# Optimization experiments

Hardware: AMD Instinct MI355X
Metric: run time of the kernel (lower is better)

The kernel has to match this reference:

```python
import jax, jax.numpy as jnp
import numpy as np

EPS = 1e-6

def _conv1x1(x, w, bias):
    # x: [b,cin,h,w], w: [cout,cin]
    y = jnp.einsum('bchw,oc->bohw', x, w)
    return y + bias[None, :, None, None]

def _maxpool2(x):
    b, c, h, w = x.shape
    return x.reshape(b, c, h // 2, 2, w // 2, 2).max(axis=(3, 5))

def _up2_align_corners(x):
    # bilinear upsample x2, align_corners=True (matches torch nn.Upsample)
    b, c, h, w = x.shape
    oh, ow = 2 * h, 2 * w
    ys = jnp.linspace(0.0, h - 1.0, oh)
    xs = jnp.linspace(0.0, w - 1.0, ow)
    y0 = jnp.floor(ys).astype(jnp.int32); y1 = jnp.minimum(y0 + 1, h - 1)
    x0 = jnp.floor(xs).astype(jnp.int32); x1 = jnp.minimum(x0 + 1, w - 1)
    ty = (ys - y0).reshape(1, 1, oh, 1)
    tx = (xs - x0).reshape(1, 1, 1, ow)
    r0 = x[:, :, y0, :]; r1 = x[:, :, y1, :]           # [b,c,oh,w]
    v00 = r0[:, :, :, x0]; v01 = r0[:, :, :, x1]       # [b,c,oh,ow]
    v10 = r1[:, :, :, x0]; v11 = r1[:, :, :, x1]
    return (1 - ty) * ((1 - tx) * v00 + tx * v01) + ty * ((1 - tx) * v10 + tx * v11)

def _norm_corr(fm):
    # fm: [b,N,N], indexed [b,p,q]; ReLU then L2-normalize over q for each p
    m = jnp.maximum(fm, 0.0)
    norm = jnp.sqrt(jnp.sum(m * m, axis=2, keepdims=True) + EPS)
    return m / norm

def setup_inputs() -> dict:
    key = jax.random.key(0)
    ks = jax.random.split(key, 8)
    d = {
        'xa': jax.random.normal(ks[0], (8, 256, 64, 64), jnp.float32),
        'xb': jax.random.normal(ks[1], (8, 256, 64, 64), jnp.float32),
        'conv_w': jax.random.normal(ks[2], (1024, 256), jnp.float32) * 0.02,
        'conv_b': jax.random.normal(ks[3], (1024,), jnp.float32) * 0.02,
        'We': jax.random.normal(ks[4], (1024, 1024), jnp.float32) * 0.02,
        'We2': jax.random.normal(ks[5], (1024, 1024), jnp.float32) * 0.02,
        'conv2_w': jax.random.normal(ks[6], (256, 1024), jnp.float32) * 0.02,
        'conv2_b': jax.random.normal(ks[7], (256,), jnp.float32) * 0.02,
    }
    return d

def reference(xa, xb, conv_w, conv_b, We, We2, conv2_w, conv2_b):
    fa = _maxpool2(_conv1x1(xa, conv_w, conv_b))   # [b,c,h,w]
    fb = _maxpool2(_conv1x1(xb, conv_w, conv_b))
    b, c, h, w = fa.shape
    N = h * w
    Fa = fa.reshape(b, c, N)                        # [b,c,N]
    Fb = fb.reshape(b, c, N)
    Fb_t = jnp.swapaxes(Fb, 1, 2)                   # [b,N,c]
    Fa_t = jnp.swapaxes(Fa, 1, 2)
    # fm[b,p,q] = (linear_e(Fb_t) @ Fa)
    fm = jnp.einsum('bpc,cd,bdq->bpq', Fb_t, We.T, Fa)
    Mab = _norm_corr(fm)                            # normalized over q per p
    fm2 = jnp.einsum('bpc,cd,bdq->bpq', Fa_t, We2.T, Fb)
    Mba = _norm_corr(fm2)
    # torch: bmm(corr.view(b,N,N), feat) with corr_flat[b,q,p] = Mn[b,p,q]
    en_a = jnp.einsum('bpq,bpk->bqk', Mab, Fa_t)    # [b,N,c]
    en_b = jnp.einsum('bpq,bpk->bqk', Mba, Fb_t)
    # faithful reinterpretation (torch .view(b,c,h,w) on a [b,N,c] tensor)
    en_a = en_a.reshape(b, c, h, w)
    en_b = en_b.reshape(b, c, h, w)
    en_a = _conv1x1(_up2_align_corners(en_a), conv2_w, conv2_b)
    en_b = _conv1x1(_up2_align_corners(en_b), conv2_w, conv2_b)
    return (en_a, en_b)
```

## Files before the change

kernel.cpp:

```cpp
#include <hip/hip_runtime.h>

typedef unsigned short u16;
typedef short bfrag __attribute__((ext_vector_type(8)));
typedef float facc  __attribute__((ext_vector_type(4)));

__device__ __forceinline__ float bf2f(u16 u) {
    union { unsigned int i; float f; } v; v.i = ((unsigned int)u) << 16; return v.f;
}
__device__ __forceinline__ u16 f2bf(float f) {
    union { float f; unsigned int i; } v; v.f = f;
    unsigned int r = v.i + 0x7FFFu + ((v.i >> 16) & 1u);
    return (u16)(r >> 16);
}

__device__ __forceinline__ void store_out(u16* p, float v)   { *p = f2bf(v); }
__device__ __forceinline__ void store_out(float* p, float v) { *p = v; }

__device__ __forceinline__ void gl2lds16(const u16* g, char* l) {
    __builtin_amdgcn_global_load_lds(
        (const __attribute__((address_space(1))) unsigned int*)g,
        (__attribute__((address_space(3))) unsigned int*)l,
        16, 0, 0);
}

__global__ void cvt4_k(const float* __restrict__ s0, u16* __restrict__ d0,
                       const float* __restrict__ s1, u16* __restrict__ d1,
                       const float* __restrict__ s2, u16* __restrict__ d2,
                       const float* __restrict__ s3, u16* __restrict__ d3) {
    int i = blockIdx.x * blockDim.x + threadIdx.x;
    if (i < 262144)        d0[i] = f2bf(s0[i]);
    else if (i < 1310720)  d1[i - 262144] = f2bf(s1[i - 262144]);
    else if (i < 2359296)  d2[i - 1310720] = f2bf(s2[i - 1310720]);
    else                   d3[i - 2359296] = f2bf(s3[i - 2359296]);
}

__global__ void transpose_in_k(const float* __restrict__ srcA,
                               const float* __restrict__ srcB,
                               u16* __restrict__ dst) {
    __shared__ u16 tile[64][65];
    const long SX = 1048576;
    const int z  = blockIdx.z;
    const int c0 = blockIdx.x * 64;
    const int r0 = blockIdx.y * 64;
    const int x  = threadIdx.x;
    const int y0 = threadIdx.y;
    const float* s = (z < 8 ? srcA : srcB) + (size_t)(z & 7) * SX;
    for (int i = 0; i < 8; ++i) {
        int r = y0 + i * 8;
        tile[r][x] = f2bf(s[(size_t)(r0 + r) * 4096 + c0 + x]);
    }
    __syncthreads();
    u16* d = dst + (size_t)z * SX;
    for (int i = 0; i < 8; ++i) {
        int c = y0 + i * 8;
        d[(size_t)(c0 + c) * 256 + r0 + x] = tile[x][c];
    }
}

template <typename OutT, int MODE, bool PAIRED>
__global__ __launch_bounds__(256)
void gemm_nt(const u16* __restrict__ A0, const u16* __restrict__ A1, long strideA,
             const u16* __restrict__ B0, const u16* __restrict__ B1, long strideBT,
             OutT* __restrict__ C, long strideC, u16* __restrict__ CT,
             const float* __restrict__ bias, int M, int N, int K) {
    constexpr bool POOL    = (MODE == 2);
    constexpr int  SMEM_SZ = POOL ? 33792 : 32768;
    __shared__ __align__(16) char smem[SMEM_SZ];
    char* As = smem;
    char* Bs = smem + 16384;

    const int gx = gridDim.x, gy = gridDim.y;
    long id = blockIdx.x + (long)gx * (blockIdx.y + (long)gy * blockIdx.z);
    long total = (long)gx * gy * gridDim.z;
    long nid = (id & 7) * (total >> 3) + (id >> 3);
    const int bx = (int)(nid % gx);
    long rr = nid / gx;
    const int by = (int)(rr % gy);
    const int b  = (int)(rr / gy);

    const int m0 = bx * 128;
    const int n0 = by * 128;

    const u16* Ab; const u16* Bb;
    if (PAIRED) {
        const int bl = b & 7;
        Ab = (b < 8 ? A0 : A1) + (size_t)bl * strideA;
        Bb = (b < 8 ? B0 : B1) + (size_t)bl * strideBT;
    } else {
        Ab = A0 + (size_t)b * strideA;
        Bb = B0 + (size_t)b * strideBT;
    }

    const int t    = threadIdx.x;
    const int lane = t & 63;
    const int w    = t >> 6;
    const int wm   = (w & 1) * 64;
    const int wn   = (w >> 1) * 64;
    const int q    = lane >> 4;
    const int ln   = lane & 15;

    const int s0 = w * 64 + lane;
    const int s1 = s0 + 256;
    const int r0s = s0 >> 2, c0s = (s0 & 3) * 8;
    const int r1s = s1 >> 2, c1s = (s1 & 3) * 8;

    const u16* pA0 = Ab + (size_t)(m0 + r0s) * K + c0s;
    const u16* pA1 = Ab + (size_t)(m0 + r1s) * K + c1s;
    const u16* pB0 = Bb + (size_t)(n0 + r0s) * K + c0s;
    const u16* pB1 = Bb + (size_t)(n0 + r1s) * K + c1s;

    facc acc[4][4];
    for (int i = 0; i < 4; ++i)
        for (int j = 0; j < 4; ++j)
            acc[i][j] = (facc)0.0f;

    const int nK = K >> 6;
    for (int kt = 0; kt < nK; ++kt) {
        const int k0 = kt << 6;
        gl2lds16(pA0 + k0,      As + s0 * 16);
        gl2lds16(pA1 + k0,      As + s1 * 16);
        gl2lds16(pA0 + k0 + 32, As + 8192 + s0 * 16);
        gl2lds16(pA1 + k0 + 32, As + 8192 + s1 * 16);
        gl2lds16(pB0 + k0,      Bs + s0 * 16);
        gl2lds16(pB1 + k0,      Bs + s1 * 16);
        gl2lds16(pB0 + k0 + 32, Bs + 8192 + s0 * 16);
        gl2lds16(pB1 + k0 + 32, Bs + 8192 + s1 * 16);
        __syncthreads();
        for (int j = 0; j < 2; ++j) {
            const char* Aj = As + j * 8192;
            const char* Bj = Bs + j * 8192;
            bfrag af[4], bfr[4];
            for (int mt = 0; mt < 4; ++mt)
                af[mt] = *reinterpret_cast<const bfrag*>(Aj + (wm + mt * 16 + ln) * 64 + q * 16);
            for (int nt = 0; nt < 4; ++nt)
                bfr[nt] = *reinterpret_cast<const bfrag*>(Bj + (wn + nt * 16 + ln) * 64 + q * 16);
            for (int mt = 0; mt < 4; ++mt)
                for (int nt = 0; nt < 4; ++nt)
                    acc[mt][nt] = __builtin_amdgcn_mfma_f32_16x16x32_bf16(af[mt], bfr[nt], acc[mt][nt], 0, 0, 0);
        }
        __syncthreads();
    }

    if (POOL) {
        u16* Cp  = (u16*)C + (size_t)b * strideC;
        float* pool0 = (float*)smem;
        float* pool1 = (float*)(smem + 16896);
        float* pb = (w >> 1) ? pool1 : pool0;
        for (int mt = 0; mt < 4; ++mt) {
            for (int nt = 0; nt < 4; ++nt) {
                for (int r = 0; r < 4; ++r) {
                    int ch = wm + mt * 16 + q * 4 + r;
                    float v = acc[mt][nt][r] + bias[m0 + ch];
                    float vm = fmaxf(v, __shfl_xor(v, 1, 64));
                    if (!(ln & 1))
                        pb[ch * 33 + ((nt * 16 + ln) >> 1)] = vm;
                }
            }
        }
        __syncthreads();
        for (int i = 0; i < 8; ++i) {
            int idx = t + i * 256;
            int ch = idx >> 4, xpp = (idx & 15) * 2;
            float v0 = fmaxf(pool0[ch * 33 + xpp],     pool1[ch * 33 + xpp]);
            float v1 = fmaxf(pool0[ch * 33 + xpp + 1], pool1[ch * 33 + xpp + 1]);
            unsigned pk = (unsigned)f2bf(v0) | ((unsigned)f2bf(v1) << 16);
            *reinterpret_cast<unsigned*>(&Cp[(size_t)(m0 + ch) * 1024 + by * 32 + xpp]) = pk;
            pool0[ch * 33 + xpp] = v0; pool0[ch * 33 + xpp + 1] = v1;
        }
        __syncthreads();
        u16* CTb = CT + (size_t)b * strideC;
        for (int i = 0; i < 8; ++i) {
            int idx = t + i * 256;
            int ch2 = (idx & 63) * 2, xp = idx >> 6;
            unsigned pk = (unsigned)f2bf(pool0[ch2 * 33 + xp]) |
                          ((unsigned)f2bf(pool0[(ch2 + 1) * 33 + xp]) << 16);
            *reinterpret_cast<unsigned*>(&CTb[(size_t)(by * 32 + xp) * 1024 + m0 + ch2]) = pk;
        }
    } else if (MODE == 0) {
        u16* Cb = (u16*)C + (size_t)b * strideC;
        u16* dump = (u16*)smem;
        for (int mt = 0; mt < 4; ++mt)
            for (int nt = 0; nt < 4; ++nt)
                for (int r = 0; r < 4; ++r)
                    dump[(wm + mt * 16 + q * 4 + r) * 128 + wn + nt * 16 + ln] = f2bf(acc[mt][nt][r]);
        __syncthreads();
        for (int i = 0; i < 8; ++i) {
            const int row = w * 32 + i * 4 + (lane >> 4);
            const uint4 v = *reinterpret_cast<const uint4*>(dump + row * 128 + (lane & 15) * 8);
            *reinterpret_cast<uint4*>(Cb + (size_t)(m0 + row) * N + n0 + (lane & 15) * 8) = v;
        }
    } else {
        OutT* Cb = C + (size_t)b * strideC;
        for (int mt = 0; mt < 4; ++mt) {
            const int rbase = m0 + wm + mt * 16 + q * 4;
            for (int nt = 0; nt < 4; ++nt) {
                const int col = n0 + wn + nt * 16 + ln;
                for (int r = 0; r < 4; ++r)
                    store_out(&Cb[(size_t)(rbase + r) * N + col], acc[mt][nt][r] + bias[rbase + r]);
            }
        }
    }
}

__global__ void norm_rk(const u16* __restrict__ fm, float* __restrict__ rinv) {
    __shared__ float red[4];
    const long row = blockIdx.x;
    const u16* p = fm + row * 1024;
    const int t = threadIdx.x;
    uint2 raw = *reinterpret_cast<const uint2*>(p + t * 4);
    float v0 = fmaxf(bf2f((u16)(raw.x & 0xFFFF)), 0.f);
    float v1 = fmaxf(bf2f((u16)(raw.x >> 16)), 0.f);
    float v2 = fmaxf(bf2f((u16)(raw.y & 0xFFFF)), 0.f);
    float v3 = fmaxf(bf2f((u16)(raw.y >> 16)), 0.f);
    float s = v0 * v0 + v1 * v1 + v2 * v2 + v3 * v3;
    for (int off = 32; off; off >>= 1) s += __shfl_down(s, off, 64);
    if ((t & 63) == 0) red[t >> 6] = s;
    __syncthreads();
    if (t == 0)
        rinv[row] = 1.0f / sqrtf(red[0] + red[1] + red[2] + red[3] + 1e-6f);
}

__global__ void transpose_scale_k(const u16* __restrict__ src,
                                  const float* __restrict__ rinv,
                                  u16* __restrict__ dst) {
    __shared__ u16 tile[64][65];
    const long S = 1048576;
    const int b  = blockIdx.z;
    const int c0 = blockIdx.x * 64;
    const int r0 = blockIdx.y * 64;
    const int x  = threadIdx.x;
    const int y0 = threadIdx.y;
    const u16* s = src + (size_t)b * S;
    const float* rv = rinv + (size_t)b * 1024;
    for (int i = 0; i < 8; ++i) {
        int r = y0 + i * 8;
        float v = fmaxf(bf2f(s[(size_t)(r0 + r) * 1024 + c0 + x]), 0.f) * rv[r0 + r];
        tile[r][x] = f2bf(v);
    }
    __syncthreads();
    u16* d = dst + (size_t)b * S;
    for (int i = 0; i < 8; ++i) {
        int c = y0 + i * 8;
        d[(size_t)(c0 + c) * 1024 + r0 + x] = tile[x][c];
    }
}

__global__ void upsample_k(const float* __restrict__ V, float* __restrict__ out, int total) {
    int idx = blockIdx.x * blockDim.x + threadIdx.x;
    if (idx >= total) return;
    int X  = idx & 63;
    int Y  = (idx >> 6) & 63;
    long bo = idx >> 12;
    const float* p = V + bo * 1024;
    const float sc = 31.0f / 63.0f;
    float ys = Y * sc;
    float xs = X * sc;
    int y0 = (int)ys; int x0 = (int)xs;
    int y1 = y0 + 1; if (y1 > 31) y1 = 31;
    int x1 = x0 + 1; if (x1 > 31) x1 = 31;
    float ty = ys - y0, tx = xs - x0;
    float v00 = p[y0 * 32 + x0], v01 = p[y0 * 32 + x1];
    float v10 = p[y1 * 32 + x0], v11 = p[y1 * 32 + x1];
    out[idx] = (1.f - ty) * ((1.f - tx) * v00 + tx * v01) + ty * ((1.f - tx) * v10 + tx * v11);
}

extern "C" void kernel_launch(void* const* d_in, const int* in_sizes, int n_in,
                              void* d_out, int out_size, void* d_ws, size_t ws_size,
                              hipStream_t stream) {
    const float* xa      = (const float*)d_in[0];
    const float* xb      = (const float*)d_in[1];
    const float* conv_w  = (const float*)d_in[2];
    const float* conv_b  = (const float*)d_in[3];
    const float* We      = (const float*)d_in[4];
    const float* We2     = (const float*)d_in[5];
    const float* conv2_w = (const float*)d_in[6];
    const float* conv2_b = (const float*)d_in[7];
    float* out = (float*)d_out;
    char* ws = (char*)d_ws;

    const long S1M = 1048576;
    const long MiB = 1048576;

    u16*   XT  = (u16*)(ws + 0);
    u16*   T1  = (u16*)(ws + 0);
    u16*   MT  = (u16*)(ws + 0);
    u16*   FA  = (u16*)(ws + 32 * MiB);
    u16*   FB  = (u16*)(ws + 48 * MiB);
    u16*   FAT = (u16*)(ws + 64 * MiB);
    u16*   FBT = (u16*)(ws + 80 * MiB);
    float* V   = (float*)(ws + 64 * MiB);
    u16*   FM  = (u16*)(ws + 96 * MiB);
    u16*   Z   = (u16*)(ws + 96 * MiB);
    u16*   CW  = (u16*)(ws + 128 * MiB);
    u16*   WE  = (u16*)(ws + 128 * MiB + 524288);
    u16*   WE2 = (u16*)(ws + 128 * MiB + 2621440);
    u16*   C2W = (u16*)(ws + 128 * MiB + 4718592);
    float* RIV = (float*)(ws + 128 * MiB + 5242880);

    const dim3 tb64(64, 8);

    cvt4_k<<<10240, 256, 0, stream>>>(conv_w, CW, We, WE, We2, WE2, conv2_w, C2W);

    transpose_in_k<<<dim3(64, 4, 16), tb64, 0, stream>>>(xa, xb, XT);

    gemm_nt<u16, 2, false><<<dim3(8, 32, 16), 256, 0, stream>>>(
        CW, CW, 0, XT, XT, S1M, FA, S1M, FAT, conv_b, 1024, 4096, 256);

    gemm_nt<u16, 0, true><<<dim3(8, 8, 16), 256, 0, stream>>>(
        FBT, FAT, S1M, WE, WE2, 0, T1, S1M, nullptr, nullptr, 1024, 1024, 1024);

    gemm_nt<u16, 0, true><<<dim3(8, 8, 16), 256, 0, stream>>>(
        T1, T1 + 8 * S1M, S1M, FAT, FBT, S1M, FM, S1M, nullptr, nullptr, 1024, 1024, 1024);

    norm_rk<<<16384, 256, 0, stream>>>(FM, RIV);

    transpose_scale_k<<<dim3(16, 16, 16), tb64, 0, stream>>>(FM, RIV, MT);

    gemm_nt<u16, 0, true><<<dim3(8, 8, 16), 256, 0, stream>>>(
        FA, FB, S1M, MT, MT + 8 * S1M, S1M, Z, S1M, nullptr, nullptr, 1024, 1024, 1024);

    gemm_nt<float, 1, false><<<dim3(2, 8, 16), 256, 0, stream>>>(
        C2W, C2W, 0, Z, Z, S1M, V, 256L * 1024, nullptr, conv2_b, 256, 1024, 1024);

    upsample_k<<<65536, 256, 0, stream>>>(V, out, 16 * 256 * 4096);
}
```

Before: 428.0 us.

## Reorder pooled-GEMM B rows so 2x2 maxpool reduces in registers via shuffles

In the fused conv+maxpool GEMM, the B-operand rows are now gathered in a permuted pixel order, so each 16-column MFMA tile holds complete 2x2 pooling windows. The pooling max is then done entirely with lane shuffles in registers, and the pooled output and its transposed copy are written straight from registers. This removes the LDS staging buffers, two block barriers and the extra shared memory in the pool epilogue. In exchange the stores become narrower and scattered (2-byte stores for C, 8-byte stores for CT), and the B loads now read non-contiguous rows.

```diff
diff --git a/kernel.cpp b/kernel.cpp
--- a/kernel.cpp
+++ b/kernel.cpp
@@ -63,9 +63,8 @@
              const u16* __restrict__ B0, const u16* __restrict__ B1, long strideBT,
              OutT* __restrict__ C, long strideC, u16* __restrict__ CT,
              const float* __restrict__ bias, int M, int N, int K) {
-    constexpr bool POOL    = (MODE == 2);
-    constexpr int  SMEM_SZ = POOL ? 33792 : 32768;
-    __shared__ __align__(16) char smem[SMEM_SZ];
+    constexpr bool POOL = (MODE == 2);
+    __shared__ __align__(16) char smem[32768];
     char* As = smem;
     char* Bs = smem + 16384;
 
@@ -104,10 +103,15 @@
     const int r0s = s0 >> 2, c0s = (s0 & 3) * 8;
     const int r1s = s1 >> 2, c1s = (s1 & 3) * 8;
 
+    const int gr0 = POOL ? ((2 * by + ((r0s >> 1) & 1)) * 64 + (r0s >> 2) * 2 + (r0s & 1))
+                         : (n0 + r0s);
+    const int gr1 = POOL ? ((2 * by + ((r1s >> 1) & 1)) * 64 + (r1s >> 2) * 2 + (r1s & 1))
+                         : (n0 + r1s);
+
     const u16* pA0 = Ab + (size_t)(m0 + r0s) * K + c0s;
     const u16* pA1 = Ab + (size_t)(m0 + r1s) * K + c1s;
-    const u16* pB0 = Bb + (size_t)(n0 + r0s) * K + c0s;
-    const u16* pB1 = Bb + (size_t)(n0 + r1s) * K + c1s;
+    const u16* pB0 = Bb + (size_t)gr0 * K + c0s;
+    const u16* pB1 = Bb + (size_t)gr1 * K + c1s;
 
     facc acc[4][4];
     for (int i = 0; i < 4; ++i)
@@ -143,38 +147,35 @@
 
     if (POOL) {
         u16* Cp  = (u16*)C + (size_t)b * strideC;
-        float* pool0 = (float*)smem;
-        float* pool1 = (float*)(smem + 16896);
-        float* pb = (w >> 1) ? pool1 : pool0;
+        u16* CTb = CT + (size_t)b * strideC;
+        const int a = ln >> 2;
         for (int mt = 0; mt < 4; ++mt) {
+            const int chb = wm + mt * 16 + q * 4;
+            float bs0 = bias[m0 + chb + 0];
+            float bs1 = bias[m0 + chb + 1];
+            float bs2 = bias[m0 + chb + 2];
+            float bs3 = bias[m0 + chb + 3];
             for (int nt = 0; nt < 4; ++nt) {
-                for (int r = 0; r < 4; ++r) {
-                    int ch = wm + mt * 16 + q * 4 + r;
-                    float v = acc[mt][nt][r] + bias[m0 + ch];
-                    float vm = fmaxf(v, __shfl_xor(v, 1, 64));
-                    if (!(ln & 1))
-                        pb[ch * 33 + ((nt * 16 + ln) >> 1)] = vm;
+                const int xp = (wn >> 2) + nt * 4 + a;
+                float p0 = acc[mt][nt][0] + bs0;
+                float p1 = acc[mt][nt][1] + bs1;
+                float p2 = acc[mt][nt][2] + bs2;
+                float p3 = acc[mt][nt][3] + bs3;
+                p0 = fmaxf(p0, __shfl_xor(p0, 1, 64)); p0 = fmaxf(p0, __shfl_xor(p0, 2, 64));
+                p1 = fmaxf(p1, __shfl_xor(p1, 1, 64)); p1 = fmaxf(p1, __shfl_xor(p1, 2, 64));
+                p2 = fmaxf(p2, __shfl_xor(p2, 1, 64)); p2 = fmaxf(p2, __shfl_xor(p2, 2, 64));
+                p3 = fmaxf(p3, __shfl_xor(p3, 1, 64)); p3 = fmaxf(p3, __shfl_xor(p3, 2, 64));
+                float s01 = (ln & 1) ? p1 : p0;
+                float s23 = (ln & 1) ? p3 : p2;
+                float sel = (ln & 2) ? s23 : s01;
+                Cp[(size_t)(m0 + chb + (ln & 3)) * 1024 + by * 32 + xp] = f2bf(sel);
+                if ((ln & 3) == 0) {
+                    uint2 pk;
+                    pk.x = (unsigned)f2bf(p0) | ((unsigned)f2bf(p1) << 16);
+                    pk.y = (unsigned)f2bf(p2) | ((unsigned)f2bf(p3) << 16);
+                    *reinterpret_cast<uint2*>(&CTb[(size_t)(by * 32 + xp) * 1024 + m0 + chb]) = pk;
                 }
             }
-        }
-        __syncthreads();
-        for (int i = 0; i < 8; ++i) {
-            int idx = t + i * 256;
-            int ch = idx >> 4, xpp = (idx & 15) * 2;
-            float v0 = fmaxf(pool0[ch * 33 + xpp],     pool1[ch * 33 + xpp]);
-            float v1 = fmaxf(pool0[ch * 33 + xpp + 1], pool1[ch * 33 + xpp + 1]);
-            unsigned pk = (unsigned)f2bf(v0) | ((unsigned)f2bf(v1) << 16);
-            *reinterpret_cast<unsigned*>(&Cp[(size_t)(m0 + ch) * 1024 + by * 32 + xpp]) = pk;
-            pool0[ch * 33 + xpp] = v0; pool0[ch * 33 + xpp + 1] = v1;
-        }
-        __syncthreads();
-        u16* CTb = CT + (size_t)b * strideC;
-        for (int i = 0; i < 8; ++i) {
-            int idx = t + i * 256;
-            int ch2 = (idx & 63) * 2, xp = idx >> 6;
-            unsigned pk = (unsigned)f2bf(pool0[ch2 * 33 + xp]) |
-                          ((unsigned)f2bf(pool0[(ch2 + 1) * 33 + xp]) << 16);
-            *reinterpret_cast<unsigned*>(&CTb[(size_t)(by * 32 + xp) * 1024 + m0 + ch2]) = pk;
         }
     } else if (MODE == 0) {
         u16* Cb = (u16*)C + (size_t)b * strideC;
```

Measured after the change: 424.0 us. About the same (-0.9%).
